# Kernel optimization log

Hardware: AMD Instinct MI355X
Metric: run time of the kernel (lower is better)

## Reference

```python
import jax, jax.numpy as jnp
import numpy as np

L, HID, NH, AD, FF = 6, 512, 8, 64, 2048
G, ST, NF, RA, RD = 8, 512, 25, 16, 20
T = G + 4 * ST  # 2056 tokens


def _ln(x, g, b, eps=1e-5):
    m = jnp.mean(x, axis=-1, keepdims=True)
    v = jnp.mean((x - m) ** 2, axis=-1, keepdims=True)
    return (x - m) * jax.lax.rsqrt(v + eps) * g + b


def _expand4(m, g):
    top = jnp.concatenate([m[:, :g, :g], jnp.repeat(m[:, :g, g:], 4, axis=2)], axis=2)
    bot = jnp.concatenate([jnp.repeat(m[:, g:, :g], 4, axis=1),
                           jnp.repeat(jnp.repeat(m[:, g:, g:], 4, axis=1), 4, axis=2)], axis=2)
    return jnp.concatenate([top, bot], axis=1)


def setup_inputs() -> dict:
    key = jax.random.key(0)
    ks = iter(jax.random.split(key, 48))
    n = lambda shape, s=0.02: (jax.random.normal(next(ks), shape, jnp.float32) * s)
    N = G + ST
    inp = {
        "obj_input": jax.random.normal(next(ks), (1, G, NF, 4), jnp.float32),
        "obj_scale": jax.random.normal(next(ks), (1, G, NF, 2), jnp.float32),
        "st_input0": jax.random.normal(next(ks), (1, ST, 10), jnp.float32),
        "rpe_a": jax.random.randint(next(ks), (1, N, N), 0, RA, jnp.int32),
        "rpe_d": jax.random.randint(next(ks), (1, N, N), 0, RD + 1, jnp.int32),
        "mask": jnp.zeros((1, N, N), jnp.float32),
        # projection heads
        "Wpg": n((4 * NF, HID)), "bpg": jnp.zeros((HID,)),
        "pg_g": jnp.ones((HID,)), "pg_b": jnp.zeros((HID,)),
        "Wps": n((2, HID)), "bps": jnp.zeros((HID,)),
        "ps_g": jnp.ones((HID,)), "ps_b": jnp.zeros((HID,)),
        # relative position embeddings
        "emb_a": n((RA, NH)), "emb_d": n((RD + 1, NH)),
        # stacked transformer layer params
        "Wq": n((L, HID, NH * AD)), "bq": jnp.zeros((L, NH * AD)),
        "Wk": n((L, HID, NH * AD)), "bk": jnp.zeros((L, NH * AD)),
        "Wv": n((L, HID, NH * AD)), "bv": jnp.zeros((L, NH * AD)),
        "Wo": n((L, NH * AD, HID)), "bo": jnp.zeros((L, HID)),
        "W1": n((L, HID, FF)), "b1": jnp.zeros((L, FF)),
        "W2": n((L, FF, HID)), "b2": jnp.zeros((L, HID)),
        "ln1_g": jnp.ones((L, HID)), "ln1_b": jnp.zeros((L, HID)),
        "ln2_g": jnp.ones((L, HID)), "ln2_b": jnp.zeros((L, HID)),
    }
    return inp


def reference(obj_input, obj_scale, st_input0, rpe_a, rpe_d, mask,
              Wpg, bpg, pg_g, pg_b, Wps, bps, ps_g, ps_b, emb_a, emb_d,
              Wq, bq, Wk, bk, Wv, bv, Wo, bo, W1, b1, W2, b2,
              ln1_g, ln1_b, ln2_g, ln2_b):
    g = obj_input.shape[1]
    # token embeddings: objects + strokes (4 points of 2 coords each)
    st = st_input0[:, :, :8].reshape(1, -1, 2)                       # [1, 4*ST, 2]
    obj_emb = jax.nn.leaky_relu(_ln(obj_input.reshape(1, g, -1) @ Wpg + bpg, pg_g, pg_b))
    st_emb = jax.nn.leaky_relu(_ln(st @ Wps + bps, ps_g, ps_b))
    x = jnp.concatenate([obj_emb, st_emb], axis=1)                   # [1, T, HID]
    t = x.shape[1]
    # relative-position bias: embed expanded angle/distance indices
    pos = emb_a[_expand4(rpe_a, g)] + emb_d[_expand4(rpe_d, g)]      # [1, T, T, NH]
    pos = jnp.transpose(pos, (0, 3, 1, 2))                           # [1, NH, T, T]
    msk = _expand4(mask, g)[:, None]                                 # [1, 1, T, T]
    inv_sqrt_d = np.float32(1.0 / np.sqrt(AD))
    for l in range(Wq.shape[0]):
        q = (x @ Wq[l] + bq[l]).reshape(1, t, NH, AD)
        k = (x @ Wk[l] + bk[l]).reshape(1, t, NH, AD)
        v = (x @ Wv[l] + bv[l]).reshape(1, t, NH, AD)
        # note: bias added BEFORE scaling, then mask (matches torch source)
        scores = (jnp.einsum('bqhd,bkhd->bhqk', q, k) + pos) * inv_sqrt_d + msk
        att = jax.nn.softmax(scores, axis=-1)
        o = jnp.einsum('bhqk,bkhd->bqhd', att, v).reshape(1, t, NH * AD)
        x = _ln(x + o @ Wo[l] + bo[l], ln1_g[l], ln1_b[l])
        h = jax.nn.leaky_relu(x @ W1[l] + b1[l])
        x = _ln(x + h @ W2[l] + b2[l], ln2_g[l], ln2_b[l])
    return x
```

## Files before the change

### kernel.cpp

```cpp
#include <hip/hip_runtime.h>
#include <math.h>

#define T_TOK 2056
#define TP 2176
#define TK 2112
#define HIDDEN 512
#define NHEAD 8
#define ADIM 64
#define FFDIM 2048
#define NLAYER 6
#define NORIG 520
#define NOBJ 8
#define NSPLIT 4
#define FSPLIT 8

typedef float f32x4 __attribute__((ext_vector_type(4)));
typedef __attribute__((__ext_vector_type__(8))) __bf16 bf16x8;

#if __has_builtin(__builtin_amdgcn_exp2f)
#define EXP2(x) __builtin_amdgcn_exp2f(x)
#else
#define EXP2(x) exp2f(x)
#endif

__device__ __forceinline__ unsigned short f2bf(float f) {
  unsigned int u = __float_as_uint(f);
  u += 0x7FFFu + ((u >> 16) & 1u);
  return (unsigned short)(u >> 16);
}
__device__ __forceinline__ float bf2f(unsigned short u) {
  return __uint_as_float(((unsigned int)u) << 16);
}


__device__ inline float blockReduceSum(float v, float* sb) {
#pragma unroll
  for (int off = 32; off > 0; off >>= 1) v += __shfl_down(v, off, 64);
  int wid = threadIdx.x >> 6;
  __syncthreads();
  if ((threadIdx.x & 63) == 0) sb[wid] = v;
  __syncthreads();
  return sb[0] + sb[1] + sb[2] + sb[3];
}


__global__ __launch_bounds__(256) void embed_kernel(
    const float* __restrict__ obj, const float* __restrict__ st0,
    const float* __restrict__ Wpg, const float* __restrict__ bpg,
    const float* __restrict__ pg_g, const float* __restrict__ pg_b,
    const float* __restrict__ Wps, const float* __restrict__ bps,
    const float* __restrict__ ps_g, const float* __restrict__ ps_b,
    float* __restrict__ x, unsigned short* __restrict__ xb)
{
  __shared__ float sb[4];
  int t = blockIdx.x;
  int j0 = threadIdx.x, j1 = threadIdx.x + 256;
  float a0, a1;
  const float *g, *b;
  if (t < NOBJ) {
    a0 = bpg[j0]; a1 = bpg[j1];
    const float* in = obj + t * 100;
    for (int i = 0; i < 100; i++) {
      float w = in[i];
      a0 += w * Wpg[i * HIDDEN + j0];
      a1 += w * Wpg[i * HIDDEN + j1];
    }
    g = pg_g; b = pg_b;
  } else {
    int tt = t - NOBJ, s = tt >> 2, p = tt & 3;
    float c0 = st0[s * 10 + p * 2], c1 = st0[s * 10 + p * 2 + 1];
    a0 = bps[j0] + c0 * Wps[j0] + c1 * Wps[HIDDEN + j0];
    a1 = bps[j1] + c0 * Wps[j1] + c1 * Wps[HIDDEN + j1];
    g = ps_g; b = ps_b;
  }
  float s1 = blockReduceSum(a0 + a1, sb);
  float s2 = blockReduceSum(a0 * a0 + a1 * a1, sb);
  float m = s1 * (1.0f / HIDDEN);
  float var = s2 * (1.0f / HIDDEN) - m * m;
  float inv = rsqrtf(var + 1e-5f);
  float y0 = (a0 - m) * inv * g[j0] + b[j0];
  float y1 = (a1 - m) * inv * g[j1] + b[j1];
  y0 = y0 >= 0.f ? y0 : 0.01f * y0;
  y1 = y1 >= 0.f ? y1 : 0.01f * y1;
  x[t * HIDDEN + j0] = y0;
  x[t * HIDDEN + j1] = y1;
  xb[t * HIDDEN + j0] = f2bf(y0);
  xb[t * HIDDEN + j1] = f2bf(y1);
}

__global__ __launch_bounds__(256) void padzero(unsigned short* __restrict__ xb) {
  int i = blockIdx.x * 256 + threadIdx.x;
  if (i < (TP - T_TOK) * HIDDEN) xb[T_TOK * HIDDEN + i] = 0;
}


__global__ __launch_bounds__(256) void posbuild(
    const int* __restrict__ rpe_a, const int* __restrict__ rpe_d,
    const float* __restrict__ emb_a, const float* __restrict__ emb_d,
    const float* __restrict__ mask, unsigned short* __restrict__ posb)
{
  int i = blockIdx.x;
  for (int j = threadIdx.x; j < NORIG; j += 256) {
    int a = rpe_a[i * NORIG + j];
    int d = rpe_d[i * NORIG + j];
    float mk = mask[i * NORIG + j];
#pragma unroll
    for (int h = 0; h < NHEAD; h++) {
      float v = ((emb_a[a * NHEAD + h] + emb_d[d * NHEAD + h]) * 0.125f + mk) * 1.44269504f;
      posb[(h * NORIG + i) * NORIG + j] = f2bf(v);
    }
  }
}


__global__ __launch_bounds__(256) void wtrans(
    const float* __restrict__ Wq, const float* __restrict__ Wk, const float* __restrict__ Wv,
    const float* __restrict__ Wo, const float* __restrict__ W1, const float* __restrict__ W2,
    unsigned short* __restrict__ Wqkvt, unsigned short* __restrict__ Wot,
    unsigned short* __restrict__ W1t, unsigned short* __restrict__ W2t)
{
  __shared__ float t[64 * 65];
  int b = blockIdx.x;
  const float* src; unsigned short* dst; int N, K, tk, tn;
  if (b < 192) {
    int m = b >> 6, bb = b & 63;
    src = m == 0 ? Wq : m == 1 ? Wk : Wv;
    dst = Wqkvt + m * 512 * 512;
    K = 512; N = 512; tk = bb & 7; tn = bb >> 3;
  } else if (b < 256) {
    int bb = b - 192; src = Wo; dst = Wot; K = 512; N = 512; tk = bb & 7; tn = bb >> 3;
  } else if (b < 512) {
    int bb = b - 256; src = W1; dst = W1t; K = 512; N = 2048; tk = bb & 7; tn = bb >> 3;
  } else {
    int bb = b - 512; src = W2; dst = W2t; K = 2048; N = 512; tk = bb & 31; tn = bb >> 5;
  }
  int k0 = tk * 64, n0 = tn * 64;
  int tid = threadIdx.x;
  int r = tid >> 2, c0 = (tid & 3) * 16;
  const float* sp = src + (k0 + r) * N + n0 + c0;
#pragma unroll
  for (int q = 0; q < 4; q++) {
    float4 f = *(const float4*)(sp + q * 4);
    t[r * 65 + c0 + q * 4 + 0] = f.x;
    t[r * 65 + c0 + q * 4 + 1] = f.y;
    t[r * 65 + c0 + q * 4 + 2] = f.z;
    t[r * 65 + c0 + q * 4 + 3] = f.w;
  }
  __syncthreads();
  unsigned short vals[16];
#pragma unroll
  for (int j = 0; j < 16; j++) vals[j] = f2bf(t[(c0 + j) * 65 + r]);
  unsigned short* dp = dst + (n0 + r) * K + k0 + c0;
  *(int4*)dp = *(int4*)&vals[0];
  *(int4*)(dp + 8) = *(int4*)&vals[8];
}


__global__ __launch_bounds__(256) void gemm_bt(
    const unsigned short* __restrict__ A, int lda,
    const unsigned short* __restrict__ Bt, int ldb, int K, int mode,
    const float* __restrict__ b0, const float* __restrict__ b1, const float* __restrict__ b2,
    unsigned short* __restrict__ d0, unsigned short* __restrict__ d1, unsigned short* __restrict__ d2,
    float* __restrict__ df, int ldc)
{
  __shared__ unsigned short As[2][64 * 40];
  __shared__ unsigned short Bs[2][128 * 40];
  const int tid = threadIdx.x;
  const int lane = tid & 63, wave = tid >> 6;
  const int l15 = lane & 15, quad = lane >> 4;
  const int rowBase = blockIdx.y * 64, colBase = blockIdx.x * 128;
  const int mw = (wave & 1) * 32, nw = (wave >> 1) * 64;
  const int sr = tid >> 2, sc = (tid & 3) * 8;
  const int zz = blockIdx.z;
  const int kLen = K / gridDim.z;
  const int kb0 = zz * kLen;
  const int nIter = kLen >> 5;
  const unsigned short* Ag0 = A + (rowBase + sr) * lda + sc;
  const unsigned short* Bg0 = Bt + (colBase + sr) * ldb + sc;
  const unsigned short* Bg1 = Bg0 + 64 * ldb;
  f32x4 acc[2][4];
#pragma unroll
  for (int i = 0; i < 2; i++)
#pragma unroll
    for (int j = 0; j < 4; j++) acc[i][j] = (f32x4){0.f, 0.f, 0.f, 0.f};

  int4 a0 = *(const int4*)(Ag0 + kb0);
  int4 g0 = *(const int4*)(Bg0 + kb0);
  int4 g1 = *(const int4*)(Bg1 + kb0);
  *(int4*)&As[0][sr * 40 + sc] = a0;
  *(int4*)&Bs[0][sr * 40 + sc] = g0;
  *(int4*)&Bs[0][(sr + 64) * 40 + sc] = g1;

  for (int it = 0; it < nIter; ++it) {
    __syncthreads();
    const int cur = it & 1, nxt = cur ^ 1;
    const bool more = (it + 1) < nIter;
    if (more) {
      int kb = kb0 + (it + 1) * 32;
      a0 = *(const int4*)(Ag0 + kb);
      g0 = *(const int4*)(Bg0 + kb);
      g1 = *(const int4*)(Bg1 + kb);
    }
    bf16x8 af[2], bfr[4];
#pragma unroll
    for (int mt = 0; mt < 2; mt++)
      af[mt] = *(const bf16x8*)&As[cur][(mw + mt * 16 + l15) * 40 + quad * 8];
#pragma unroll
    for (int nt = 0; nt < 4; nt++)
      bfr[nt] = *(const bf16x8*)&Bs[cur][(nw + nt * 16 + l15) * 40 + quad * 8];
#pragma unroll
    for (int mt = 0; mt < 2; mt++)
#pragma unroll
      for (int nt = 0; nt < 4; nt++)
        acc[mt][nt] = __builtin_amdgcn_mfma_f32_16x16x32_bf16(af[mt], bfr[nt], acc[mt][nt], 0, 0, 0);
    if (more) {
      *(int4*)&As[nxt][sr * 40 + sc] = a0;
      *(int4*)&Bs[nxt][sr * 40 + sc] = g0;
      *(int4*)&Bs[nxt][(sr + 64) * 40 + sc] = g1;
    }
  }

  float* dfz = df + (size_t)zz * TP * ldc;
#pragma unroll
  for (int mt = 0; mt < 2; mt++) {
#pragma unroll
    for (int nt = 0; nt < 4; nt++) {
#pragma unroll
      for (int r = 0; r < 4; r++) {
        int row = rowBase + mw + mt * 16 + quad * 4 + r;
        int col = colBase + nw + nt * 16 + l15;
        float v = acc[mt][nt][r];
        if (mode == 0) {
          int seg = col >> 9, cc = col & 511;
          const float* bs = seg == 0 ? b0 : seg == 1 ? b1 : b2;
          unsigned short* dst = seg == 0 ? d0 : seg == 1 ? d1 : d2;
          int hd = cc >> 6, d = cc & 63;
          float t = v + bs[cc];
          if (seg == 0) t *= 0.180336880111f;
          dst[(hd * TP + row) * 64 + d] = f2bf(t);
        } else if (mode == 1) {
          dfz[row * ldc + col] = v;
        } else {
          float t = v + b0[col];
          t = t >= 0.f ? t : 0.01f * t;
          d0[row * ldc + col] = f2bf(t);
        }
      }
    }
  }
}


__global__ __launch_bounds__(256) void vt_trans(
    const unsigned short* __restrict__ vh, unsigned short* __restrict__ vt)
{
  __shared__ unsigned short t[64 * 72];
  int kt = blockIdx.x, h = blockIdx.y;
  int tid = threadIdx.x;
  int r0 = tid >> 3, cs = (tid & 7) * 8;
  const unsigned short* src = vh + (h * TP + kt * 64 + r0) * 64 + cs;
  *(int4*)&t[r0 * 72 + cs] = *(const int4*)src;
  *(int4*)&t[(r0 + 32) * 72 + cs] = *(const int4*)(src + 32 * 64);
  __syncthreads();
  int d = tid >> 2, c0 = (tid & 3) * 16;
  unsigned short vals[16];
#pragma unroll
  for (int j = 0; j < 16; j++) vals[j] = t[(c0 + j) * 72 + d];
  unsigned short* dst = vt + (h * 64 + d) * TK + kt * 64 + c0;
  *(int4*)dst = *(int4*)&vals[0];
  *(int4*)(dst + 8) = *(int4*)&vals[8];
}


__global__ __launch_bounds__(256) void flash_attn(
    const unsigned short* __restrict__ qh, const unsigned short* __restrict__ kh,
    const unsigned short* __restrict__ vt, const unsigned short* __restrict__ posb,
    unsigned short* __restrict__ Opart, float* __restrict__ lbuf)
{
  __shared__ unsigned short Ks[64 * 72];
  __shared__ unsigned short Vs[80 * 88];
  __shared__ unsigned short Ps[64 * 72];
  __shared__ float pt[24 * 24];
  const int tid = threadIdx.x;
  const int lane = tid & 63, wave = tid >> 6;
  const int l15 = lane & 15, quad = lane >> 4;
  const int qt = blockIdx.x, h = blockIdx.y, z = blockIdx.z;
  const int q0 = qt * 64;
  const int qrow = q0 + wave * 16 + l15;
  const unsigned short* qbp = qh + (h * TP + qrow) * 64;
  bf16x8 qf0 = *(const bf16x8*)(qbp + quad * 8);
  bf16x8 qf1 = *(const bf16x8*)(qbp + 32 + quad * 8);
  f32x4 O[5];
#pragma unroll
  for (int nt = 0; nt < 5; nt++) O[nt] = (f32x4){0.f, 0.f, 0.f, 0.f};
  for (int idx = tid; idx < 16 * 88; idx += 256) {
    int rr = idx / 88, cc = idx - rr * 88;
    Vs[(64 + rr) * 88 + cc] = (rr == 0) ? 0x3F80 : 0;
  }
  const int oq0 = q0 < 8 ? q0 : 8 + ((q0 - 8) >> 2);
  const int qe = min(q0 + 63, T_TOK - 1);
  const int nq = (qe < 8 ? qe : 8 + ((qe - 8) >> 2)) - oq0 + 1;
  int myq[4];
#pragma unroll
  for (int r = 0; r < 4; r++) {
    int qr = q0 + wave * 16 + quad * 4 + r;
    myq[r] = (qr < 8 ? qr : 8 + ((qr - 8) >> 2)) - oq0;
  }
  const int sr = tid >> 3, sc = (tid & 7) * 8;
  const unsigned short* kgb = kh + (h * TP + sr) * 64 + sc;
  const unsigned short* vgb = vt + (h * 64 + sr) * TK + sc;
  const int ptrow = tid >> 3, ptc0 = (tid & 7) * 3;
  const bool prok = (ptrow < 24) && (ptrow < nq);

  const int nT = (33 - z + FSPLIT - 1) / FSPLIT;
  int kb = z * 64;
  int4 kv0 = *(const int4*)(kgb + kb * 64);
  int4 kv1 = *(const int4*)(kgb + (kb + 32) * 64);
  int4 vv0 = *(const int4*)(vgb + kb);
  int4 vv1 = *(const int4*)(vgb + 32 * TK + kb);
  float ppf0, ppf1, ppf2;
  {
    int ok0n = kb < 8 ? kb : 8 + ((kb - 8) >> 2);
    int ken = min(kb + 63, T_TOK - 1);
    int nkn = (ken < 8 ? ken : 8 + ((ken - 8) >> 2)) - ok0n + 1;
    const unsigned short* prow = posb + (h * NORIG + oq0 + ptrow) * NORIG + ok0n;
    ppf0 = (prok && ptc0 + 0 < nkn) ? bf2f(prow[ptc0 + 0]) : 0.f;
    ppf1 = (prok && ptc0 + 1 < nkn) ? bf2f(prow[ptc0 + 1]) : 0.f;
    ppf2 = (prok && ptc0 + 2 < nkn) ? bf2f(prow[ptc0 + 2]) : 0.f;
  }

  for (int i = 0; i < nT; ++i) {
    const int kbCur = kb;
    const int ok0c = kbCur < 8 ? kbCur : 8 + ((kbCur - 8) >> 2);
    __syncthreads();
    *(int4*)&Ks[sr * 72 + sc] = kv0;
    *(int4*)&Ks[(sr + 32) * 72 + sc] = kv1;
    *(int4*)&Vs[sr * 88 + sc] = vv0;
    *(int4*)&Vs[(sr + 32) * 88 + sc] = vv1;
    if (ptrow < 24) {
      pt[ptrow * 24 + ptc0 + 0] = ppf0;
      pt[ptrow * 24 + ptc0 + 1] = ppf1;
      pt[ptrow * 24 + ptc0 + 2] = ppf2;
    }
    __syncthreads();
    kb += FSPLIT * 64;
    if (i + 1 < nT) {
      kv0 = *(const int4*)(kgb + kb * 64);
      kv1 = *(const int4*)(kgb + (kb + 32) * 64);
      vv0 = *(const int4*)(vgb + kb);
      vv1 = *(const int4*)(vgb + 32 * TK + kb);
      int ok0n = kb < 8 ? kb : 8 + ((kb - 8) >> 2);
      int ken = min(kb + 63, T_TOK - 1);
      int nkn = (ken < 8 ? ken : 8 + ((ken - 8) >> 2)) - ok0n + 1;
      const unsigned short* prow = posb + (h * NORIG + oq0 + ptrow) * NORIG + ok0n;
      ppf0 = (prok && ptc0 + 0 < nkn) ? bf2f(prow[ptc0 + 0]) : 0.f;
      ppf1 = (prok && ptc0 + 1 < nkn) ? bf2f(prow[ptc0 + 1]) : 0.f;
      ppf2 = (prok && ptc0 + 2 < nkn) ? bf2f(prow[ptc0 + 2]) : 0.f;
    }
    f32x4 S[4];
#pragma unroll
    for (int nt = 0; nt < 4; nt++) S[nt] = (f32x4){0.f, 0.f, 0.f, 0.f};
#pragma unroll
    for (int nt = 0; nt < 4; nt++) {
      bf16x8 kf0 = *(const bf16x8*)&Ks[(nt * 16 + l15) * 72 + quad * 8];
      bf16x8 kf1 = *(const bf16x8*)&Ks[(nt * 16 + l15) * 72 + 32 + quad * 8];
      S[nt] = __builtin_amdgcn_mfma_f32_16x16x32_bf16(qf0, kf0, S[nt], 0, 0, 0);
      S[nt] = __builtin_amdgcn_mfma_f32_16x16x32_bf16(qf1, kf1, S[nt], 0, 0, 0);
    }
    int okp[4]; bool cval[4];
#pragma unroll
    for (int nt = 0; nt < 4; nt++) {
      int c = kbCur + nt * 16 + l15;
      cval[nt] = c < T_TOK;
      okp[nt] = (c < 8 ? c : 8 + ((c - 8) >> 2)) - ok0c;
    }
#pragma unroll
    for (int r = 0; r < 4; r++) {
      int pr = wave * 16 + quad * 4 + r;
#pragma unroll
      for (int nt = 0; nt < 4; nt++) {
        float a = cval[nt] ? fminf(S[nt][r] + pt[myq[r] * 24 + okp[nt]], 86.f) : -1e30f;
        Ps[pr * 72 + nt * 16 + l15] = f2bf(EXP2(a));
      }
    }
    bf16x8 pa0 = *(const bf16x8*)&Ps[(wave * 16 + l15) * 72 + quad * 8];
    bf16x8 pa1 = *(const bf16x8*)&Ps[(wave * 16 + l15) * 72 + 32 + quad * 8];
#pragma unroll
    for (int nt = 0; nt < 5; nt++) {
      bf16x8 vb0 = *(const bf16x8*)&Vs[(nt * 16 + l15) * 88 + quad * 8];
      bf16x8 vb1 = *(const bf16x8*)&Vs[(nt * 16 + l15) * 88 + 32 + quad * 8];
      O[nt] = __builtin_amdgcn_mfma_f32_16x16x32_bf16(pa0, vb0, O[nt], 0, 0, 0);
      O[nt] = __builtin_amdgcn_mfma_f32_16x16x32_bf16(pa1, vb1, O[nt], 0, 0, 0);
    }
  }
#pragma unroll
  for (int r = 0; r < 4; r++) {
    int orow = q0 + wave * 16 + quad * 4 + r;
    size_t base = ((size_t)(z * NHEAD + h) * TK + orow);
    if (l15 == 0) lbuf[base] = O[4][r];
#pragma unroll
    for (int nt = 0; nt < 4; nt++)
      Opart[base * 64 + nt * 16 + l15] = f2bf(O[nt][r]);
  }
}


__global__ __launch_bounds__(256) void flash_merge(
    const unsigned short* __restrict__ Opart, const float* __restrict__ lbuf,
    unsigned short* __restrict__ ob)
{
  int idx = blockIdx.x * 256 + threadIdx.x;
  if (idx >= T_TOK * HIDDEN) return;
  int row = idx >> 9, c = idx & 511;
  int h = c >> 6, d = c & 63;
  float num = 0.f, den = 0.f;
#pragma unroll
  for (int s = 0; s < FSPLIT; s++) {
    size_t base = ((size_t)(s * NHEAD + h) * TK + row);
    den += lbuf[base];
    num += bf2f(Opart[base * 64 + d]);
  }
  ob[idx] = f2bf(num / den);
}


__global__ __launch_bounds__(256) void ln_residual4(
    float* __restrict__ x, const float* __restrict__ parts,
    const float* __restrict__ bias,
    const float* __restrict__ g, const float* __restrict__ b,
    unsigned short* __restrict__ xb)
{
  __shared__ float sb[4];
  int row = blockIdx.x;
  int j0 = threadIdx.x, j1 = threadIdx.x + 256;
  int base = row * HIDDEN;
  const size_t ss = (size_t)TP * HIDDEN;
  float v0 = x[base + j0] + bias[j0] + parts[base + j0] + parts[ss + base + j0]
           + parts[2 * ss + base + j0] + parts[3 * ss + base + j0];
  float v1 = x[base + j1] + bias[j1] + parts[base + j1] + parts[ss + base + j1]
           + parts[2 * ss + base + j1] + parts[3 * ss + base + j1];
  float s1 = blockReduceSum(v0 + v1, sb);
  float s2 = blockReduceSum(v0 * v0 + v1 * v1, sb);
  float m = s1 * (1.0f / HIDDEN);
  float var = s2 * (1.0f / HIDDEN) - m * m;
  float inv = rsqrtf(var + 1e-5f);
  float y0 = (v0 - m) * inv * g[j0] + b[j0];
  float y1 = (v1 - m) * inv * g[j1] + b[j1];
  x[base + j0] = y0;
  x[base + j1] = y1;
  xb[base + j0] = f2bf(y0);
  xb[base + j1] = f2bf(y1);
}

__global__ __launch_bounds__(256) void copy_out(
    const float4* __restrict__ src, float4* __restrict__ dst, int n4)
{
  int i = blockIdx.x * 256 + threadIdx.x;
  if (i < n4) dst[i] = src[i];
}


extern "C" void kernel_launch(void* const* d_in, const int* in_sizes, int n_in,
                              void* d_out, int out_size, void* d_ws, size_t ws_size,
                              hipStream_t stream) {
  const float* obj   = (const float*)d_in[0];
  const float* st0   = (const float*)d_in[2];
  const int*   rpe_a = (const int*)d_in[3];
  const int*   rpe_d = (const int*)d_in[4];
  const float* mask  = (const float*)d_in[5];
  const float* Wpg = (const float*)d_in[6];  const float* bpg = (const float*)d_in[7];
  const float* pg_g = (const float*)d_in[8]; const float* pg_b = (const float*)d_in[9];
  const float* Wps = (const float*)d_in[10]; const float* bps = (const float*)d_in[11];
  const float* ps_g = (const float*)d_in[12];const float* ps_b = (const float*)d_in[13];
  const float* emb_a = (const float*)d_in[14];
  const float* emb_d = (const float*)d_in[15];
  const float* Wq = (const float*)d_in[16]; const float* bq = (const float*)d_in[17];
  const float* Wk = (const float*)d_in[18]; const float* bk = (const float*)d_in[19];
  const float* Wv = (const float*)d_in[20]; const float* bv = (const float*)d_in[21];
  const float* Wo = (const float*)d_in[22]; const float* bo = (const float*)d_in[23];
  const float* W1 = (const float*)d_in[24]; const float* b1 = (const float*)d_in[25];
  const float* W2 = (const float*)d_in[26]; const float* b2 = (const float*)d_in[27];
  const float* ln1_g = (const float*)d_in[28]; const float* ln1_b = (const float*)d_in[29];
  const float* ln2_g = (const float*)d_in[30]; const float* ln2_b = (const float*)d_in[31];

  char* p = (char*)d_ws;
  auto alloc = [&](size_t bytes) { char* q = p; p += (bytes + 255) & ~(size_t)255; return q; };
  float*          x      = (float*)alloc((size_t)T_TOK * HIDDEN * 4);
  unsigned short* xb     = (unsigned short*)alloc((size_t)TP * HIDDEN * 2);
  char*           u1     = (char*)alloc((size_t)TP * FFDIM * 2);
  unsigned short* qhb    = (unsigned short*)u1;
  unsigned short* khb    = qhb + (size_t)NHEAD * TP * ADIM;
  unsigned short* vhb    = khb + (size_t)NHEAD * TP * ADIM;
  unsigned short* vtb    = vhb + (size_t)NHEAD * TP * ADIM;
  unsigned short* hb     = (unsigned short*)u1;
  unsigned short* ob     = (unsigned short*)alloc((size_t)TP * HIDDEN * 2);
  size_t opartB = (size_t)FSPLIT * NHEAD * TK * ADIM * 2;
  size_t partsB = (size_t)NSPLIT * TP * HIDDEN * 4;
  size_t u2B = opartB + (size_t)FSPLIT * NHEAD * TK * 4;
  if (partsB > u2B) u2B = partsB;
  char*           u2     = (char*)alloc(u2B);
  unsigned short* Opart  = (unsigned short*)u2;
  float*          lbb    = (float*)(u2 + opartB);
  float*          parts  = (float*)u2;
  unsigned short* posb   = (unsigned short*)alloc((size_t)NHEAD * NORIG * NORIG * 2);
  size_t perLayerW = ((size_t)1536 * 512 + 512 * 512 + 2048 * 512 + 512 * 2048) * 2;
  size_t baseUsed = (size_t)(p - (char*)d_ws);
  bool hoist = (baseUsed + 6 * perLayerW + 2048) <= ws_size;
  int nWsets = hoist ? 6 : 1;
  unsigned short* Wsets = (unsigned short*)alloc(perLayerW * nWsets);
  if ((size_t)(p - (char*)d_ws) > ws_size) return;

  auto wq_t = [&](int l) { return Wsets + (hoist ? l : 0) * (perLayerW / 2); };
  auto wo_t = [&](int l) { return wq_t(l) + (size_t)1536 * 512; };
  auto w1_t = [&](int l) { return wo_t(l) + (size_t)512 * 512; };
  auto w2_t = [&](int l) { return w1_t(l) + (size_t)2048 * 512; };

  float* out = (float*)d_out;

  embed_kernel<<<T_TOK, 256, 0, stream>>>(obj, st0, Wpg, bpg, pg_g, pg_b,
                                          Wps, bps, ps_g, ps_b, x, xb);
  padzero<<<((TP - T_TOK) * HIDDEN + 255) / 256, 256, 0, stream>>>(xb);
  posbuild<<<NORIG, 256, 0, stream>>>(rpe_a, rpe_d, emb_a, emb_d, mask, posb);
  if (hoist) {
    for (int l = 0; l < NLAYER; l++)
      wtrans<<<768, 256, 0, stream>>>(
          Wq + l * 512 * 512, Wk + l * 512 * 512, Wv + l * 512 * 512,
          Wo + l * 512 * 512, W1 + l * 512 * 2048, W2 + l * 2048 * 512,
          wq_t(l), wo_t(l), w1_t(l), w2_t(l));
  }

  for (int l = 0; l < NLAYER; l++) {
    if (!hoist) {
      wtrans<<<768, 256, 0, stream>>>(
          Wq + l * 512 * 512, Wk + l * 512 * 512, Wv + l * 512 * 512,
          Wo + l * 512 * 512, W1 + l * 512 * 2048, W2 + l * 2048 * 512,
          wq_t(l), wo_t(l), w1_t(l), w2_t(l));
    }
    gemm_bt<<<dim3(12, 34, 1), 256, 0, stream>>>(
        xb, HIDDEN, wq_t(l), HIDDEN, HIDDEN, 0,
        bq + l * 512, bk + l * 512, bv + l * 512, qhb, khb, vhb, nullptr, 0);
    vt_trans<<<dim3(33, 8), 256, 0, stream>>>(vhb, vtb);
    flash_attn<<<dim3(33, 8, FSPLIT), 256, 0, stream>>>(
        qhb, khb, vtb, posb, Opart, lbb);
    flash_merge<<<(T_TOK * HIDDEN + 255) / 256, 256, 0, stream>>>(Opart, lbb, ob);
    gemm_bt<<<dim3(4, 34, NSPLIT), 256, 0, stream>>>(
        ob, HIDDEN, wo_t(l), HIDDEN, HIDDEN, 1,
        nullptr, nullptr, nullptr, nullptr, nullptr, nullptr, parts, HIDDEN);
    ln_residual4<<<T_TOK, 256, 0, stream>>>(x, parts, bo + l * 512,
                                            ln1_g + l * 512, ln1_b + l * 512, xb);
    gemm_bt<<<dim3(16, 34, 1), 256, 0, stream>>>(
        xb, HIDDEN, w1_t(l), HIDDEN, HIDDEN, 2,
        b1 + l * 2048, nullptr, nullptr, hb, nullptr, nullptr, nullptr, FFDIM);
    gemm_bt<<<dim3(4, 34, NSPLIT), 256, 0, stream>>>(
        hb, FFDIM, w2_t(l), FFDIM, FFDIM, 1,
        nullptr, nullptr, nullptr, nullptr, nullptr, nullptr, parts, HIDDEN);
    ln_residual4<<<T_TOK, 256, 0, stream>>>(x, parts, b2 + l * 512,
                                            ln2_g + l * 512, ln2_b + l * 512, xb);
  }

  int n4 = T_TOK * HIDDEN / 4;
  copy_out<<<(n4 + 255) / 256, 256, 0, stream>>>((const float4*)x, (float4*)out, n4);
}
```

Measured before the change: 960.8 us.

## Enlarge flash attention query tile, halve KV split, deepen GEMM prefetch

The flash attention kernel now handles 128 query rows per block, with each wave computing two 16-row tiles, so every K/V tile loaded into shared memory is reused twice as much. The KV split factor drops from 8 to 4, which shrinks the partial output buffers and the work in the merge kernel. The GEMM main loop is restructured into a two-stage register prefetch with explicit LDS double buffering, and P conversion uses packed bf16 conversion. The trade-off is fewer blocks for attention (17x8x4), higher register pressure, and more shared memory per block, all of which can reduce occupancy.

```diff
diff --git a/kernel.cpp b/kernel.cpp
--- a/kernel.cpp
+++ b/kernel.cpp
@@ -12,7 +12,7 @@
 #define NORIG 520
 #define NOBJ 8
 #define NSPLIT 4
-#define FSPLIT 8
+#define FSPLIT 4
 
 typedef float f32x4 __attribute__((ext_vector_type(4)));
 typedef __attribute__((__ext_vector_type__(8))) __bf16 bf16x8;
@@ -30,6 +30,16 @@
 }
 __device__ __forceinline__ float bf2f(unsigned short u) {
   return __uint_as_float(((unsigned int)u) << 16);
+}
+__device__ __forceinline__ unsigned pk2bf(float a, float b) {
+#if __has_builtin(__builtin_amdgcn_cvt_pk_bf16_f32)
+  auto v = __builtin_amdgcn_cvt_pk_bf16_f32(a, b);
+  unsigned u;
+  __builtin_memcpy(&u, &v, 4);
+  return u;
+#else
+  return (unsigned)f2bf(a) | ((unsigned)f2bf(b) << 16);
+#endif
 }
 
 
@@ -184,23 +194,7 @@
 #pragma unroll
     for (int j = 0; j < 4; j++) acc[i][j] = (f32x4){0.f, 0.f, 0.f, 0.f};
 
-  int4 a0 = *(const int4*)(Ag0 + kb0);
-  int4 g0 = *(const int4*)(Bg0 + kb0);
-  int4 g1 = *(const int4*)(Bg1 + kb0);
-  *(int4*)&As[0][sr * 40 + sc] = a0;
-  *(int4*)&Bs[0][sr * 40 + sc] = g0;
-  *(int4*)&Bs[0][(sr + 64) * 40 + sc] = g1;
-
-  for (int it = 0; it < nIter; ++it) {
-    __syncthreads();
-    const int cur = it & 1, nxt = cur ^ 1;
-    const bool more = (it + 1) < nIter;
-    if (more) {
-      int kb = kb0 + (it + 1) * 32;
-      a0 = *(const int4*)(Ag0 + kb);
-      g0 = *(const int4*)(Bg0 + kb);
-      g1 = *(const int4*)(Bg1 + kb);
-    }
+  auto compute = [&](int cur) {
     bf16x8 af[2], bfr[4];
 #pragma unroll
     for (int mt = 0; mt < 2; mt++)
@@ -213,11 +207,47 @@
 #pragma unroll
       for (int nt = 0; nt < 4; nt++)
         acc[mt][nt] = __builtin_amdgcn_mfma_f32_16x16x32_bf16(af[mt], bfr[nt], acc[mt][nt], 0, 0, 0);
-    if (more) {
-      *(int4*)&As[nxt][sr * 40 + sc] = a0;
-      *(int4*)&Bs[nxt][sr * 40 + sc] = g0;
-      *(int4*)&Bs[nxt][(sr + 64) * 40 + sc] = g1;
-    }
+  };
+
+  int4 A0, G00, G10, A1, G01, G11;
+  A0  = *(const int4*)(Ag0 + kb0);
+  G00 = *(const int4*)(Bg0 + kb0);
+  G10 = *(const int4*)(Bg1 + kb0);
+  *(int4*)&As[0][sr * 40 + sc] = A0;
+  *(int4*)&Bs[0][sr * 40 + sc] = G00;
+  *(int4*)&Bs[0][(sr + 64) * 40 + sc] = G10;
+  A1  = *(const int4*)(Ag0 + kb0 + 32);
+  G01 = *(const int4*)(Bg0 + kb0 + 32);
+  G11 = *(const int4*)(Bg1 + kb0 + 32);
+  A0  = *(const int4*)(Ag0 + kb0 + 64);
+  G00 = *(const int4*)(Bg0 + kb0 + 64);
+  G10 = *(const int4*)(Bg1 + kb0 + 64);
+
+  for (int ip = 0; ip < nIter; ip += 2) {
+    __syncthreads();
+    *(int4*)&As[1][sr * 40 + sc] = A1;
+    *(int4*)&Bs[1][sr * 40 + sc] = G01;
+    *(int4*)&Bs[1][(sr + 64) * 40 + sc] = G11;
+    if (ip + 3 < nIter) {
+      int kb = kb0 + (ip + 3) * 32;
+      A1  = *(const int4*)(Ag0 + kb);
+      G01 = *(const int4*)(Bg0 + kb);
+      G11 = *(const int4*)(Bg1 + kb);
+    }
+    compute(0);
+    __syncthreads();
+    if (ip + 2 < nIter) {
+      *(int4*)&As[0][sr * 40 + sc] = A0;
+      *(int4*)&Bs[0][sr * 40 + sc] = G00;
+      *(int4*)&Bs[0][(sr + 64) * 40 + sc] = G10;
+    }
+    if (ip + 4 < nIter) {
+      int kb = kb0 + (ip + 4) * 32;
+      A0  = *(const int4*)(Ag0 + kb);
+      G00 = *(const int4*)(Bg0 + kb);
+      G10 = *(const int4*)(Bg1 + kb);
+    }
+    compute(1);
   }
 
   float* dfz = df + (size_t)zz * TP * ldc;
@@ -279,38 +309,44 @@
 {
   __shared__ unsigned short Ks[64 * 72];
   __shared__ unsigned short Vs[80 * 88];
-  __shared__ unsigned short Ps[64 * 72];
-  __shared__ float pt[24 * 24];
+  __shared__ unsigned short Ps[128 * 72];
+  __shared__ float pt[40 * 24];
   const int tid = threadIdx.x;
   const int lane = tid & 63, wave = tid >> 6;
   const int l15 = lane & 15, quad = lane >> 4;
   const int qt = blockIdx.x, h = blockIdx.y, z = blockIdx.z;
-  const int q0 = qt * 64;
-  const int qrow = q0 + wave * 16 + l15;
-  const unsigned short* qbp = qh + (h * TP + qrow) * 64;
-  bf16x8 qf0 = *(const bf16x8*)(qbp + quad * 8);
-  bf16x8 qf1 = *(const bf16x8*)(qbp + 32 + quad * 8);
-  f32x4 O[5];
-#pragma unroll
-  for (int nt = 0; nt < 5; nt++) O[nt] = (f32x4){0.f, 0.f, 0.f, 0.f};
+  const int q0 = qt * 128;
+  const int wbase = wave * 32;
+  bf16x8 qf[2][2];
+#pragma unroll
+  for (int mt = 0; mt < 2; mt++) {
+    const unsigned short* qbp = qh + (h * TP + q0 + wbase + mt * 16 + l15) * 64;
+    qf[mt][0] = *(const bf16x8*)(qbp + quad * 8);
+    qf[mt][1] = *(const bf16x8*)(qbp + 32 + quad * 8);
+  }
+  f32x4 O[2][5];
+#pragma unroll
+  for (int mt = 0; mt < 2; mt++)
+#pragma unroll
+    for (int nt = 0; nt < 5; nt++) O[mt][nt] = (f32x4){0.f, 0.f, 0.f, 0.f};
   for (int idx = tid; idx < 16 * 88; idx += 256) {
     int rr = idx / 88, cc = idx - rr * 88;
     Vs[(64 + rr) * 88 + cc] = (rr == 0) ? 0x3F80 : 0;
   }
   const int oq0 = q0 < 8 ? q0 : 8 + ((q0 - 8) >> 2);
-  const int qe = min(q0 + 63, T_TOK - 1);
+  const int qe = min(q0 + 127, T_TOK - 1);
   const int nq = (qe < 8 ? qe : 8 + ((qe - 8) >> 2)) - oq0 + 1;
-  int myq[4];
-#pragma unroll
-  for (int r = 0; r < 4; r++) {
-    int qr = q0 + wave * 16 + quad * 4 + r;
-    myq[r] = (qr < 8 ? qr : 8 + ((qr - 8) >> 2)) - oq0;
-  }
+  int myq[2][4];
+#pragma unroll
+  for (int mt = 0; mt < 2; mt++)
+#pragma unroll
+    for (int r = 0; r < 4; r++) {
+      int qr = q0 + wbase + mt * 16 + quad * 4 + r;
+      myq[mt][r] = (qr < 8 ? qr : 8 + ((qr - 8) >> 2)) - oq0;
+    }
   const int sr = tid >> 3, sc = (tid & 7) * 8;
   const unsigned short* kgb = kh + (h * TP + sr) * 64 + sc;
   const unsigned short* vgb = vt + (h * 64 + sr) * TK + sc;
-  const int ptrow = tid >> 3, ptc0 = (tid & 7) * 3;
-  const bool prok = (ptrow < 24) && (ptrow < nq);
 
   const int nT = (33 - z + FSPLIT - 1) / FSPLIT;
   int kb = z * 64;
@@ -318,18 +354,20 @@
   int4 kv1 = *(const int4*)(kgb + (kb + 32) * 64);
   int4 vv0 = *(const int4*)(vgb + kb);
   int4 vv1 = *(const int4*)(vgb + 32 * TK + kb);
-  float ppf0, ppf1, ppf2;
+  float ppf[4];
   {
     int ok0n = kb < 8 ? kb : 8 + ((kb - 8) >> 2);
     int ken = min(kb + 63, T_TOK - 1);
     int nkn = (ken < 8 ? ken : 8 + ((ken - 8) >> 2)) - ok0n + 1;
-    const unsigned short* prow = posb + (h * NORIG + oq0 + ptrow) * NORIG + ok0n;
-    ppf0 = (prok && ptc0 + 0 < nkn) ? bf2f(prow[ptc0 + 0]) : 0.f;
-    ppf1 = (prok && ptc0 + 1 < nkn) ? bf2f(prow[ptc0 + 1]) : 0.f;
-    ppf2 = (prok && ptc0 + 2 < nkn) ? bf2f(prow[ptc0 + 2]) : 0.f;
-  }
-
-  for (int i = 0; i < nT; ++i) {
+#pragma unroll
+    for (int u = 0; u < 4; u++) {
+      int e = tid + 256 * u;
+      int i = e / 24, j = e - i * 24;
+      ppf[u] = (i < nq && j < nkn) ? bf2f(posb[(h * NORIG + oq0 + i) * NORIG + ok0n + j]) : 0.f;
+    }
+  }
+
+  for (int it = 0; it < nT; ++it) {
     const int kbCur = kb;
     const int ok0c = kbCur < 8 ? kbCur : 8 + ((kbCur - 8) >> 2);
     __syncthreads();
@@ -337,14 +375,15 @@
     *(int4*)&Ks[(sr + 32) * 72 + sc] = kv1;
     *(int4*)&Vs[sr * 88 + sc] = vv0;
     *(int4*)&Vs[(sr + 32) * 88 + sc] = vv1;
-    if (ptrow < 24) {
-      pt[ptrow * 24 + ptc0 + 0] = ppf0;
-      pt[ptrow * 24 + ptc0 + 1] = ppf1;
-      pt[ptrow * 24 + ptc0 + 2] = ppf2;
+#pragma unroll
+    for (int u = 0; u < 4; u++) {
+      int e = tid + 256 * u;
+      int i = e / 24, j = e - i * 24;
+      if (i < 40) pt[i * 24 + j] = ppf[u];
     }
     __syncthreads();
     kb += FSPLIT * 64;
-    if (i + 1 < nT) {
+    if (it + 1 < nT) {
       kv0 = *(const int4*)(kgb + kb * 64);
       kv1 = *(const int4*)(kgb + (kb + 32) * 64);
       vv0 = *(const int4*)(vgb + kb);
@@ -352,20 +391,27 @@
       int ok0n = kb < 8 ? kb : 8 + ((kb - 8) >> 2);
       int ken = min(kb + 63, T_TOK - 1);
       int nkn = (ken < 8 ? ken : 8 + ((ken - 8) >> 2)) - ok0n + 1;
-      const unsigned short* prow = posb + (h * NORIG + oq0 + ptrow) * NORIG + ok0n;
-      ppf0 = (prok && ptc0 + 0 < nkn) ? bf2f(prow[ptc0 + 0]) : 0.f;
-      ppf1 = (prok && ptc0 + 1 < nkn) ? bf2f(prow[ptc0 + 1]) : 0.f;
-      ppf2 = (prok && ptc0 + 2 < nkn) ? bf2f(prow[ptc0 + 2]) : 0.f;
-    }
-    f32x4 S[4];
-#pragma unroll
-    for (int nt = 0; nt < 4; nt++) S[nt] = (f32x4){0.f, 0.f, 0.f, 0.f};
+#pragma unroll
+      for (int u = 0; u < 4; u++) {
+        int e = tid + 256 * u;
+        int i = e / 24, j = e - i * 24;
+        ppf[u] = (i < nq && j < nkn) ? bf2f(posb[(h * NORIG + oq0 + i) * NORIG + ok0n + j]) : 0.f;
+      }
+    }
+    f32x4 S[2][4];
+#pragma unroll
+    for (int mt = 0; mt < 2; mt++)
+#pragma unroll
+      for (int nt = 0; nt < 4; nt++) S[mt][nt] = (f32x4){0.f, 0.f, 0.f, 0.f};
 #pragma unroll
     for (int nt = 0; nt < 4; nt++) {
       bf16x8 kf0 = *(const bf16x8*)&Ks[(nt * 16 + l15) * 72 + quad * 8];
       bf16x8 kf1 = *(const bf16x8*)&Ks[(nt * 16 + l15) * 72 + 32 + quad * 8];
-      S[nt] = __builtin_amdgcn_mfma_f32_16x16x32_bf16(qf0, kf0, S[nt], 0, 0, 0);
-      S[nt] = __builtin_amdgcn_mfma_f32_16x16x32_bf16(qf1, kf1, S[nt], 0, 0, 0);
+#pragma unroll
+      for (int mt = 0; mt < 2; mt++) {
+        S[mt][nt] = __builtin_amdgcn_mfma_f32_16x16x32_bf16(qf[mt][0], kf0, S[mt][nt], 0, 0, 0);
+        S[mt][nt] = __builtin_amdgcn_mfma_f32_16x16x32_bf16(qf[mt][1], kf1, S[mt][nt], 0, 0, 0);
+      }
     }
     int okp[4]; bool cval[4];
 #pragma unroll
@@ -375,32 +421,54 @@
       okp[nt] = (c < 8 ? c : 8 + ((c - 8) >> 2)) - ok0c;
     }
 #pragma unroll
-    for (int r = 0; r < 4; r++) {
-      int pr = wave * 16 + quad * 4 + r;
+    for (int mt = 0; mt < 2; mt++) {
+      const int prb = wbase + mt * 16 + quad * 4;
 #pragma unroll
       for (int nt = 0; nt < 4; nt++) {
-        float a = cval[nt] ? fminf(S[nt][r] + pt[myq[r] * 24 + okp[nt]], 86.f) : -1e30f;
-        Ps[pr * 72 + nt * 16 + l15] = f2bf(EXP2(a));
+        const int cidx = nt * 16 + l15;
+        float e0, e1, e2, e3;
+        {
+          float a0 = cval[nt] ? fminf(S[mt][nt][0] + pt[myq[mt][0] * 24 + okp[nt]], 86.f) : -1e30f;
+          float a1 = cval[nt] ? fminf(S[mt][nt][1] + pt[myq[mt][1] * 24 + okp[nt]], 86.f) : -1e30f;
+          float a2 = cval[nt] ? fminf(S[mt][nt][2] + pt[myq[mt][2] * 24 + okp[nt]], 86.f) : -1e30f;
+          float a3 = cval[nt] ? fminf(S[mt][nt][3] + pt[myq[mt][3] * 24 + okp[nt]], 86.f) : -1e30f;
+          e0 = EXP2(a0); e1 = EXP2(a1); e2 = EXP2(a2); e3 = EXP2(a3);
+        }
+        unsigned u01 = pk2bf(e0, e1), u23 = pk2bf(e2, e3);
+        Ps[(prb + 0) * 72 + cidx] = (unsigned short)u01;
+        Ps[(prb + 1) * 72 + cidx] = (unsigned short)(u01 >> 16);
+        Ps[(prb + 2) * 72 + cidx] = (unsigned short)u23;
+        Ps[(prb + 3) * 72 + cidx] = (unsigned short)(u23 >> 16);
       }
     }
-    bf16x8 pa0 = *(const bf16x8*)&Ps[(wave * 16 + l15) * 72 + quad * 8];
-    bf16x8 pa1 = *(const bf16x8*)&Ps[(wave * 16 + l15) * 72 + 32 + quad * 8];
+    bf16x8 pa[2][2];
+#pragma unroll
+    for (int mt = 0; mt < 2; mt++) {
+      pa[mt][0] = *(const bf16x8*)&Ps[(wbase + mt * 16 + l15) * 72 + quad * 8];
+      pa[mt][1] = *(const bf16x8*)&Ps[(wbase + mt * 16 + l15) * 72 + 32 + quad * 8];
+    }
 #pragma unroll
     for (int nt = 0; nt < 5; nt++) {
       bf16x8 vb0 = *(const bf16x8*)&Vs[(nt * 16 + l15) * 88 + quad * 8];
       bf16x8 vb1 = *(const bf16x8*)&Vs[(nt * 16 + l15) * 88 + 32 + quad * 8];
-      O[nt] = __builtin_amdgcn_mfma_f32_16x16x32_bf16(pa0, vb0, O[nt], 0, 0, 0);
-      O[nt] = __builtin_amdgcn_mfma_f32_16x16x32_bf16(pa1, vb1, O[nt], 0, 0, 0);
-    }
-  }
-#pragma unroll
-  for (int r = 0; r < 4; r++) {
-    int orow = q0 + wave * 16 + quad * 4 + r;
-    size_t base = ((size_t)(z * NHEAD + h) * TK + orow);
-    if (l15 == 0) lbuf[base] = O[4][r];
-#pragma unroll
-    for (int nt = 0; nt < 4; nt++)
-      Opart[base * 64 + nt * 16 + l15] = f2bf(O[nt][r]);
+#pragma unroll
+      for (int mt = 0; mt < 2; mt++) {
+        O[mt][nt] = __builtin_amdgcn_mfma_f32_16x16x32_bf16(pa[mt][0], vb0, O[mt][nt], 0, 0, 0);
+        O[mt][nt] = __builtin_amdgcn_mfma_f32_16x16x32_bf16(pa[mt][1], vb1, O[mt][nt], 0, 0, 0);
+      }
+    }
+  }
+#pragma unroll
+  for (int mt = 0; mt < 2; mt++) {
+#pragma unroll
+    for (int r = 0; r < 4; r++) {
+      int orow = q0 + wbase + mt * 16 + quad * 4 + r;
+      size_t base = ((size_t)(z * NHEAD + h) * TP + orow);
+      if (l15 == 0) lbuf[base] = O[mt][4][r];
+#pragma unroll
+      for (int nt = 0; nt < 4; nt++)
+        Opart[base * 64 + nt * 16 + l15] = f2bf(O[mt][nt][r]);
+    }
   }
 }
 
@@ -416,7 +484,7 @@
   float num = 0.f, den = 0.f;
 #pragma unroll
   for (int s = 0; s < FSPLIT; s++) {
-    size_t base = ((size_t)(s * NHEAD + h) * TK + row);
+    size_t base = ((size_t)(s * NHEAD + h) * TP + row);
     den += lbuf[base];
     num += bf2f(Opart[base * 64 + d]);
   }
@@ -494,9 +562,9 @@
   unsigned short* vtb    = vhb + (size_t)NHEAD * TP * ADIM;
   unsigned short* hb     = (unsigned short*)u1;
   unsigned short* ob     = (unsigned short*)alloc((size_t)TP * HIDDEN * 2);
-  size_t opartB = (size_t)FSPLIT * NHEAD * TK * ADIM * 2;
+  size_t opartB = (size_t)FSPLIT * NHEAD * TP * ADIM * 2;
   size_t partsB = (size_t)NSPLIT * TP * HIDDEN * 4;
-  size_t u2B = opartB + (size_t)FSPLIT * NHEAD * TK * 4;
+  size_t u2B = opartB + (size_t)FSPLIT * NHEAD * TP * 4;
   if (partsB > u2B) u2B = partsB;
   char*           u2     = (char*)alloc(u2B);
   unsigned short* Opart  = (unsigned short*)u2;
@@ -540,7 +608,7 @@
         xb, HIDDEN, wq_t(l), HIDDEN, HIDDEN, 0,
         bq + l * 512, bk + l * 512, bv + l * 512, qhb, khb, vhb, nullptr, 0);
     vt_trans<<<dim3(33, 8), 256, 0, stream>>>(vhb, vtb);
-    flash_attn<<<dim3(33, 8, FSPLIT), 256, 0, stream>>>(
+    flash_attn<<<dim3(17, 8, FSPLIT), 256, 0, stream>>>(
         qhb, khb, vtb, posb, Opart, lbb);
     flash_merge<<<(T_TOK * HIDDEN + 255) / 256, 256, 0, stream>>>(Opart, lbb, ob);
     gemm_bt<<<dim3(4, 34, NSPLIT), 256, 0, stream>>>(
```

New measurement: 1.084 ms. 1.13x slower.

## Use direct global-to-LDS loads with XOR swizzle in GEMM; pack bf16 converts in attention

Applied to the files above, without the earlier changes.

The GEMM now uses global_load_lds to copy tiles straight from global memory into LDS, skipping the register staging and the separate LDS stores. The unpadded 32-wide rows use an XOR swizzle on the k-chunk index to avoid bank conflicts. The attention softmax-exp loop uses a packed hardware f32-to-bf16 conversion for pairs of values. Risks: the next-buffer direct load is issued after only one barrier and nothing explicitly waits on its completion (vmcnt) before the following barrier, so correctness depends on compiler-inserted waits.

```diff
diff --git a/kernel.cpp b/kernel.cpp
--- a/kernel.cpp
+++ b/kernel.cpp
@@ -30,6 +30,22 @@
 }
 __device__ __forceinline__ float bf2f(unsigned short u) {
   return __uint_as_float(((unsigned int)u) << 16);
+}
+__device__ __forceinline__ unsigned pk2bf(float a, float b) {
+#if __has_builtin(__builtin_amdgcn_cvt_pk_bf16_f32)
+  auto v = __builtin_amdgcn_cvt_pk_bf16_f32(a, b);
+  unsigned u;
+  __builtin_memcpy(&u, &v, 4);
+  return u;
+#else
+  return (unsigned)f2bf(a) | ((unsigned)f2bf(b) << 16);
+#endif
+}
+
+__device__ __forceinline__ void gl_lds16(const void* g, void* l) {
+  __builtin_amdgcn_global_load_lds(
+      (const __attribute__((address_space(1))) void*)g,
+      (__attribute__((address_space(3))) void*)l, 16, 0, 0);
 }
 
 
@@ -163,61 +179,64 @@
     unsigned short* __restrict__ d0, unsigned short* __restrict__ d1, unsigned short* __restrict__ d2,
     float* __restrict__ df, int ldc)
 {
-  __shared__ unsigned short As[2][64 * 40];
-  __shared__ unsigned short Bs[2][128 * 40];
+  __shared__ unsigned short As[2][64 * 32];
+  __shared__ unsigned short Bs[2][128 * 32];
   const int tid = threadIdx.x;
   const int lane = tid & 63, wave = tid >> 6;
   const int l15 = lane & 15, quad = lane >> 4;
   const int rowBase = blockIdx.y * 64, colBase = blockIdx.x * 128;
   const int mw = (wave & 1) * 32, nw = (wave >> 1) * 64;
-  const int sr = tid >> 2, sc = (tid & 3) * 8;
   const int zz = blockIdx.z;
   const int kLen = K / gridDim.z;
   const int kb0 = zz * kLen;
   const int nIter = kLen >> 5;
-  const unsigned short* Ag0 = A + (rowBase + sr) * lda + sc;
-  const unsigned short* Bg0 = Bt + (colBase + sr) * ldb + sc;
-  const unsigned short* Bg1 = Bg0 + 64 * ldb;
+  const int srow = tid >> 2;
+  const int kchunk = (tid & 3) ^ ((srow >> 1) & 3);
+  const unsigned short* Ag  = A  + (size_t)(rowBase + srow) * lda + kb0 + kchunk * 8;
+  const unsigned short* Bg0 = Bt + (size_t)(colBase + srow) * ldb + kb0 + kchunk * 8;
+  const unsigned short* Bg1 = Bg0 + (size_t)64 * ldb;
+  int aoff[2], boff[4];
+#pragma unroll
+  for (int mt = 0; mt < 2; mt++) {
+    int row = mw + mt * 16 + l15;
+    aoff[mt] = row * 32 + ((quad ^ ((row >> 1) & 3)) * 8);
+  }
+#pragma unroll
+  for (int nt = 0; nt < 4; nt++) {
+    int row = nw + nt * 16 + l15;
+    boff[nt] = row * 32 + ((quad ^ ((row >> 1) & 3)) * 8);
+  }
   f32x4 acc[2][4];
 #pragma unroll
   for (int i = 0; i < 2; i++)
 #pragma unroll
     for (int j = 0; j < 4; j++) acc[i][j] = (f32x4){0.f, 0.f, 0.f, 0.f};
 
-  int4 a0 = *(const int4*)(Ag0 + kb0);
-  int4 g0 = *(const int4*)(Bg0 + kb0);
-  int4 g1 = *(const int4*)(Bg1 + kb0);
-  *(int4*)&As[0][sr * 40 + sc] = a0;
-  *(int4*)&Bs[0][sr * 40 + sc] = g0;
-  *(int4*)&Bs[0][(sr + 64) * 40 + sc] = g1;
+  gl_lds16(Ag,  (unsigned short*)As[0] + tid * 8);
+  gl_lds16(Bg0, (unsigned short*)Bs[0] + tid * 8);
+  gl_lds16(Bg1, (unsigned short*)Bs[0] + 2048 + tid * 8);
 
   for (int it = 0; it < nIter; ++it) {
+    const int cur = it & 1, nxt = cur ^ 1;
     __syncthreads();
-    const int cur = it & 1, nxt = cur ^ 1;
-    const bool more = (it + 1) < nIter;
-    if (more) {
-      int kb = kb0 + (it + 1) * 32;
-      a0 = *(const int4*)(Ag0 + kb);
-      g0 = *(const int4*)(Bg0 + kb);
-      g1 = *(const int4*)(Bg1 + kb);
+    if (it + 1 < nIter) {
+      int koff = (it + 1) * 32;
+      gl_lds16(Ag + koff,  (unsigned short*)As[nxt] + tid * 8);
+      gl_lds16(Bg0 + koff, (unsigned short*)Bs[nxt] + tid * 8);
+      gl_lds16(Bg1 + koff, (unsigned short*)Bs[nxt] + 2048 + tid * 8);
     }
     bf16x8 af[2], bfr[4];
 #pragma unroll
     for (int mt = 0; mt < 2; mt++)
-      af[mt] = *(const bf16x8*)&As[cur][(mw + mt * 16 + l15) * 40 + quad * 8];
+      af[mt] = *(const bf16x8*)&As[cur][aoff[mt]];
 #pragma unroll
     for (int nt = 0; nt < 4; nt++)
-      bfr[nt] = *(const bf16x8*)&Bs[cur][(nw + nt * 16 + l15) * 40 + quad * 8];
+      bfr[nt] = *(const bf16x8*)&Bs[cur][boff[nt]];
 #pragma unroll
     for (int mt = 0; mt < 2; mt++)
 #pragma unroll
       for (int nt = 0; nt < 4; nt++)
         acc[mt][nt] = __builtin_amdgcn_mfma_f32_16x16x32_bf16(af[mt], bfr[nt], acc[mt][nt], 0, 0, 0);
-    if (more) {
-      *(int4*)&As[nxt][sr * 40 + sc] = a0;
-      *(int4*)&Bs[nxt][sr * 40 + sc] = g0;
-      *(int4*)&Bs[nxt][(sr + 64) * 40 + sc] = g1;
-    }
   }
 
   float* dfz = df + (size_t)zz * TP * ldc;
@@ -329,7 +348,7 @@
     ppf2 = (prok && ptc0 + 2 < nkn) ? bf2f(prow[ptc0 + 2]) : 0.f;
   }
 
-  for (int i = 0; i < nT; ++i) {
+  for (int it = 0; it < nT; ++it) {
     const int kbCur = kb;
     const int ok0c = kbCur < 8 ? kbCur : 8 + ((kbCur - 8) >> 2);
     __syncthreads();
@@ -344,7 +363,7 @@
     }
     __syncthreads();
     kb += FSPLIT * 64;
-    if (i + 1 < nT) {
+    if (it + 1 < nT) {
       kv0 = *(const int4*)(kgb + kb * 64);
       kv1 = *(const int4*)(kgb + (kb + 32) * 64);
       vv0 = *(const int4*)(vgb + kb);
@@ -374,14 +393,20 @@
       cval[nt] = c < T_TOK;
       okp[nt] = (c < 8 ? c : 8 + ((c - 8) >> 2)) - ok0c;
     }
-#pragma unroll
-    for (int r = 0; r < 4; r++) {
-      int pr = wave * 16 + quad * 4 + r;
-#pragma unroll
-      for (int nt = 0; nt < 4; nt++) {
-        float a = cval[nt] ? fminf(S[nt][r] + pt[myq[r] * 24 + okp[nt]], 86.f) : -1e30f;
-        Ps[pr * 72 + nt * 16 + l15] = f2bf(EXP2(a));
-      }
+    const int prb = wave * 16 + quad * 4;
+#pragma unroll
+    for (int nt = 0; nt < 4; nt++) {
+      const int cidx = nt * 16 + l15;
+      float a0 = cval[nt] ? fminf(S[nt][0] + pt[myq[0] * 24 + okp[nt]], 86.f) : -1e30f;
+      float a1 = cval[nt] ? fminf(S[nt][1] + pt[myq[1] * 24 + okp[nt]], 86.f) : -1e30f;
+      float a2 = cval[nt] ? fminf(S[nt][2] + pt[myq[2] * 24 + okp[nt]], 86.f) : -1e30f;
+      float a3 = cval[nt] ? fminf(S[nt][3] + pt[myq[3] * 24 + okp[nt]], 86.f) : -1e30f;
+      unsigned u01 = pk2bf(EXP2(a0), EXP2(a1));
+      unsigned u23 = pk2bf(EXP2(a2), EXP2(a3));
+      Ps[(prb + 0) * 72 + cidx] = (unsigned short)u01;
+      Ps[(prb + 1) * 72 + cidx] = (unsigned short)(u01 >> 16);
+      Ps[(prb + 2) * 72 + cidx] = (unsigned short)u23;
+      Ps[(prb + 3) * 72 + cidx] = (unsigned short)(u23 >> 16);
     }
     bf16x8 pa0 = *(const bf16x8*)&Ps[(wave * 16 + l15) * 72 + quad * 8];
     bf16x8 pa1 = *(const bf16x8*)&Ps[(wave * 16 + l15) * 72 + 32 + quad * 8];
```

New measurement: 957.8 us. No clear change (-0.3%).
